# Kernel optimization log

Hardware: AMD Instinct MI355X
Metric: run time of the kernel (lower is better)

The kernel has to match this reference:

```python
import jax, jax.numpy as jnp
import numpy as np

NUM_CLASS = 3
SCORE_THRESH = 0.1
NMS_THRESH = 0.25
PRE = 512    # NMS_PRE_MAXSIZE (reduced from 4096 for memory; same algorithm)
POST = 100   # NMS_POST_MAXSIZE
EPS = 1e-8


def _cross(a, b):
    return a[..., 0] * b[..., 1] - a[..., 1] * b[..., 0]


def _corners(box):
    # box: (7,) = (x, y, z, dx, dy, dz, heading) -> BEV corners (4,2), CCW
    x, y, dx, dy, r = box[0], box[1], box[3], box[4], box[6]
    c, s = jnp.cos(r), jnp.sin(r)
    lx = jnp.array([0.5, -0.5, -0.5, 0.5]) * dx
    ly = jnp.array([0.5, 0.5, -0.5, -0.5]) * dy
    return jnp.stack([x + lx * c - ly * s, y + lx * s + ly * c], axis=-1)


def _in_box(pts, box):
    # pts (P,2): point-in-rotated-rect test in the box frame
    px, py = pts[:, 0] - box[0], pts[:, 1] - box[1]
    c, s = jnp.cos(box[6]), jnp.sin(box[6])
    u = px * c + py * s
    v = -px * s + py * c
    return (jnp.abs(u) <= box[3] * 0.5 + 1e-5) & (jnp.abs(v) <= box[4] * 0.5 + 1e-5)


def _bev_inter_area(ba, bb):
    # Exact rotated-rect intersection area (same construction as the CUDA
    # iou3d kernel: inside corners + edge intersections, angle-sorted shoelace).
    ca, cb = _corners(ba), _corners(bb)
    pa, ra = ca, jnp.roll(ca, -1, 0) - ca       # edges of a
    pb, rb = cb, jnp.roll(cb, -1, 0) - cb       # edges of b
    d = _cross(ra[:, None, :], rb[None, :, :])  # (4,4)
    dsafe = jnp.where(jnp.abs(d) > EPS, d, 1.0)
    qp = pb[None, :, :] - pa[:, None, :]
    t = _cross(qp, rb[None, :, :]) / dsafe
    u = _cross(qp, ra[:, None, :]) / dsafe
    vi = (jnp.abs(d) > EPS) & (t >= 0.0) & (t <= 1.0) & (u >= 0.0) & (u <= 1.0)
    ip = pa[:, None, :] + t[..., None] * ra[:, None, :]  # (4,4,2)
    pts = jnp.concatenate([ca, cb, ip.reshape(16, 2)], 0)          # (24,2)
    val = jnp.concatenate([_in_box(ca, bb), _in_box(cb, ba), vi.reshape(16)], 0)
    cnt = val.sum()
    ctr = (pts * val[:, None]).sum(0) / jnp.maximum(cnt, 1)
    ang = jnp.where(val, jnp.arctan2(pts[:, 1] - ctr[1], pts[:, 0] - ctr[0]), 1e9)
    o = jnp.argsort(ang)
    ps, vs = pts[o], val[o]
    ps = jnp.where(vs[:, None], ps, ps[0])  # collapse invalid onto first valid pt
    area = 0.5 * jnp.abs(_cross(ps, jnp.roll(ps, -1, 0)).sum())
    return jnp.where(cnt >= 3, area, 0.0)


def _iou3d(ba, bb):
    inter = _bev_inter_area(ba, bb)
    zt = jnp.minimum(ba[2] + ba[5] * 0.5, bb[2] + bb[5] * 0.5)
    zb = jnp.maximum(ba[2] - ba[5] * 0.5, bb[2] - bb[5] * 0.5)
    i3 = inter * jnp.maximum(zt - zb, 0.0)
    va = ba[3] * ba[4] * ba[5]
    vb = bb[3] * bb[4] * bb[5]
    return i3 / jnp.maximum(va + vb - i3, EPS)


_iou_mat = jax.vmap(jax.vmap(_iou3d, (None, 0)), (0, None))


def _nms(scores, boxes):
    # scores (K,) sorted descending; greedy suppression in score order
    valid = scores >= SCORE_THRESH
    iou = _iou_mat(boxes, boxes)  # (K,K)

    def body(sup, inp):
        row, v, i = inp
        keep = v & jnp.logical_not(sup[i])
        sup = sup | (keep & (row > NMS_THRESH))
        return sup, keep

    K = scores.shape[0]
    _, keep = jax.lax.scan(body, jnp.zeros((K,), bool), (iou, valid, jnp.arange(K)))
    return keep


def _post_one(cls_logits, boxes):
    # multi_classes_nms path: cls_preds_normalized=False -> sigmoid
    scores = jax.nn.sigmoid(cls_logits)  # (N, NUM_CLASS)
    out_b, out_s, out_l = [], [], []
    for k in range(NUM_CLASS):
        s = jnp.where(scores[:, k] >= SCORE_THRESH, scores[:, k], -1.0)
        top_s, idx = jax.lax.top_k(s, PRE)
        b = boxes[idx]
        keep = _nms(top_s, b)
        ks = jnp.where(keep, top_s, -1.0)
        os_, oi = jax.lax.top_k(ks, POST)
        ov = os_ >= SCORE_THRESH
        out_b.append(jnp.where(ov[:, None], b[oi], 0.0))
        out_s.append(jnp.where(ov, os_, 0.0))
        out_l.append((k + 1) * ov.astype(jnp.int32))  # final_labels = k + 1
    return (jnp.concatenate(out_b, 0), jnp.concatenate(out_s, 0),
            jnp.concatenate(out_l, 0))


def setup_inputs() -> dict:
    key = jax.random.key(0)
    k1, k2 = jax.random.split(key)
    B, N = 2, 100000
    batch_cls_preds = jax.random.normal(k1, (B, N, NUM_CLASS), dtype=jnp.float32)
    u = jax.random.uniform(k2, (B, N, 7), dtype=jnp.float32)
    x = u[..., 0] * 70.0
    y = u[..., 1] * 80.0 - 40.0
    z = u[..., 2] * 2.0 - 1.0
    dx = u[..., 3] * 3.0 + 1.5
    dy = u[..., 4] * 1.5 + 1.2
    dz = u[..., 5] * 1.0 + 1.3
    r = u[..., 6] * 2.0 * np.pi - np.pi
    batch_box_preds = jnp.stack([x, y, z, dx, dy, dz, r], axis=-1)
    return {"batch_cls_preds": batch_cls_preds, "batch_box_preds": batch_box_preds}


def reference(batch_cls_preds, batch_box_preds):
    # returns per-batch padded (pred_boxes (B, 3*POST, 7), pred_scores, pred_labels);
    # invalid slots are zeroed (label 0 == no detection)
    return jax.vmap(_post_one)(batch_cls_preds, batch_box_preds)
```

## Files before the change

### kernel.cpp

```cpp
#include <hip/hip_runtime.h>
#include <cstdint>

#define NCLS 3
#define NPTS 100000
#define NB 2
#define PRE 512
#define POST 100
#define SCORE_TH 0.1f
#define NMS_TH 0.25
#define CAP 1024
#define NBINS 384
#define XBIN_SH 16
#define XBIN_OFF (0xBFC00000u >> XBIN_SH)
#define XMARG 2e-3f
#define NPROB (NB * NCLS)
#define CPB 4
#define NKB 25
#define BUFREG 1024
#define BUFSZ (NKB * BUFREG)
#define NCELL 36
#define GEOP 21
#define NRB 1024
#define RB_OFF (0xBF400000u >> 12)


__device__ __forceinline__ uint32_t score_key(float x)
{
    double sd = 1.0 / (1.0 + exp(-(double)x));
    float s = (float)sd;
    if (!(s >= SCORE_TH)) s = -1.0f;
    uint32_t u = __float_as_uint(s);
    return (u & 0x80000000u) ? ~u : (u | 0x80000000u);
}

__device__ __forceinline__ int xbin(float x)
{
    uint32_t u = __float_as_uint(x);
    uint32_t key = (u & 0x80000000u) ? ~u : (u | 0x80000000u);
    int b = (int)(key >> XBIN_SH) - (int)XBIN_OFF;
    return b < 0 ? 0 : (b > NBINS - 1 ? NBINS - 1 : b);
}

__global__ __launch_bounds__(1024) void hist_stage_kernel(
    const float* __restrict__ cls, uint32_t* __restrict__ hist_part,
    uint32_t* __restrict__ blkcnt, unsigned long long* __restrict__ buf)
{
    __shared__ uint32_t lh[NCLS][NBINS];
    __shared__ uint32_t lcnt3[NCLS];
    const int tid = threadIdx.x;
    for (int t = tid; t < NCLS * NBINS; t += 1024) ((uint32_t*)lh)[t] = 0;
    if (tid < NCLS) lcnt3[tid] = 0;
    __syncthreads();

    const int b = blockIdx.x / NKB, kb = blockIdx.x % NKB;
    const float* base = cls + (size_t)b * NPTS * NCLS;
    #pragma unroll
    for (int c = 0; c < CPB; ++c) {
        int i = (kb * CPB + c) * 1024 + tid;
        if (i < NPTS) {
            const float* cp = base + (size_t)i * NCLS;
            #pragma unroll
            for (int k = 0; k < NCLS; ++k) {
                float x = cp[k];
                int bn = xbin(x);
                if (bn > 0) atomicAdd(&lh[k][bn], 1u);
                if (xbin(x + XMARG) >= 1) {
                    uint32_t slot = atomicAdd(&lcnt3[k], 1u);
                    if (slot < BUFREG)
                        buf[(size_t)(b * NCLS + k) * BUFSZ + kb * BUFREG + slot]
                            = ((unsigned long long)__float_as_uint(x) << 32)
                            | (uint32_t)i;
                }
            }
        }
    }
    __syncthreads();
    for (int t = tid; t < NCLS * NBINS; t += 1024) {
        int k = t / NBINS, bin = t % NBINS;
        hist_part[((size_t)(b * NCLS + k) * NBINS + bin) * NKB + kb]
            = lh[k][bin];
    }
    if (tid < NCLS) {
        uint32_t c = lcnt3[tid];
        blkcnt[(b * NKB + kb) * NCLS + tid] = c < BUFREG ? c : BUFREG;
    }
}

__global__ __launch_bounds__(1024) void cell_kernel(
    const float* __restrict__ boxes, const uint32_t* __restrict__ hist_part,
    const uint32_t* __restrict__ blkcnt,
    const unsigned long long* __restrict__ buf,
    uint32_t* __restrict__ cand_idx, float* __restrict__ cand_score,
    unsigned long long* __restrict__ mask)
{
    const int blk = blockIdx.x;
    const int p = blk / NCELL;
    const int b = p / NCLS, k = p % NCLS;
    int cc = blk % NCELL;
    int wi = 0;
    while (cc >= 8 - wi) { cc -= 8 - wi; ++wi; }
    const int wj = wi + cc;
    const int tid = threadIdx.x;
    const int lane = tid & 63;
    const int wv = tid >> 6;

    __shared__ unsigned long long skey[CAP];
    __shared__ unsigned long long skey2[CAP];
    __shared__ uint32_t sbins[NBINS];
    __shared__ uint32_t sblk[NKB];
    __shared__ uint32_t rhist[NRB + 1];
    __shared__ uint32_t rcnt[NRB];
    __shared__ double geo[128][GEOP];
    __shared__ float scx[128], scy[128];
    __shared__ float sczlo[128], sczhi[128], scrad[128];
    __shared__ uint32_t lcnt;

    for (int t = tid; t < 128 * GEOP; t += 1024) ((double*)geo)[t] = 0.0;
    rhist[tid] = 0;
    rcnt[tid] = 0;
    if (tid == 0) { rhist[NRB] = 0; lcnt = 0; }
    if (tid < 128) {
        scx[tid] = 0.0f; scy[tid] = 0.0f;
        sczlo[tid] = 0.0f; sczhi[tid] = 0.0f; scrad[tid] = 0.0f;
    }
    if (wi == 0 && wj == 0 && tid < PRE) {
        cand_idx[p * PRE + tid] = 0;
        cand_score[p * PRE + tid] = -1.0f;
    }
    if (tid < NKB) sblk[tid] = blkcnt[(b * NKB + tid) * NCLS + k];
    if (tid < NBINS) {
        const uint32_t* bp2 = hist_part
            + ((size_t)(b * NCLS + k) * NBINS + tid) * NKB;
        uint32_t s = 0;
        #pragma unroll 5
        for (int kb = 0; kb < NKB; ++kb)
            s += bp2[kb];
        sbins[tid] = s;
    }
    __syncthreads();

    int pb;
    {
        int pbw = -1;
        uint32_t carry = 0;
        #pragma unroll
        for (int c = 5; c >= 0; --c) {
            uint32_t v = sbins[c * 64 + lane];
            #pragma unroll
            for (int off = 1; off < 64; off <<= 1) {
                uint32_t o = __shfl_down(v, off);
                v += (lane + off < 64) ? o : 0u;
            }
            uint32_t full = v + carry;
            unsigned long long bal = __ballot(full >= PRE);
            if (pbw < 0 && bal)
                pbw = c * 64 + (63 - __clzll((long long)bal));
            carry += (uint32_t)__shfl((int)v, 0);
        }
        pb = pbw < 1 ? 1 : pbw;
    }

    {
        const int q = tid >> 8;
        const int slot0 = tid & 255;
        for (int r0 = 0; r0 < NKB; r0 += 4) {
            const int r = r0 + q;
            if (r < NKB) {
                const uint32_t c_r = sblk[r];
                const unsigned long long* R =
                    buf + (size_t)p * BUFSZ + r * BUFREG;
                for (uint32_t t = (uint32_t)slot0; t < c_r; t += 256) {
                    unsigned long long e = R[t];
                    float x = __uint_as_float((uint32_t)(e >> 32));
                    uint32_t i = (uint32_t)e;
                    if (xbin(x + XMARG) >= pb) {
                        uint32_t kk = score_key(x);
                        uint32_t slot = atomicAdd(&lcnt, 1u);
                        if (slot < CAP)
                            skey[slot] = ((unsigned long long)kk << 32)
                                       | (uint32_t)(~i);
                    }
                }
            }
        }
    }
    __syncthreads();
    const int cnt = (int)(lcnt < CAP ? lcnt : CAP);

    unsigned long long mykey = (tid < cnt) ? skey[tid] : 0ull;
    int myrb = 0;
    if (tid < cnt) {
        uint32_t kk = (uint32_t)(mykey >> 32);
        int v = (int)(kk >> 12) - (int)RB_OFF;
        myrb = v < 0 ? 0 : (v > NRB - 1 ? NRB - 1 : v);
        atomicAdd(&rhist[myrb], 1u);
    }
    __syncthreads();

    if (wv == 0) {
        uint32_t carry = 0;
        for (int c = (NRB / 64) - 1; c >= 0; --c) {
            uint32_t v = rhist[c * 64 + lane];
            uint32_t sfx = v;
            #pragma unroll
            for (int off = 1; off < 64; off <<= 1) {
                uint32_t o = __shfl_down(sfx, off);
                sfx += (lane + off < 64) ? o : 0u;
            }
            rhist[c * 64 + lane] = sfx + carry;
            carry += (uint32_t)__shfl((int)sfx, 0);
        }
    }
    __syncthreads();

    int mylo = 0;
    if (tid < cnt) {
        mylo = (int)rhist[myrb + 1];
        uint32_t off = atomicAdd(&rcnt[myrb], 1u);
        skey2[mylo + off] = mykey;
    }
    __syncthreads();

    int rank = 0;
    if (tid < cnt) {
        const int hi2 = (int)rhist[myrb];
        int c2 = 0;
        for (int t = mylo; t < hi2; ++t)
            c2 += (skey2[t] > mykey) ? 1 : 0;
        rank = mylo + c2;
    }

    if (tid < cnt) {
        uint32_t idx = ~((uint32_t)mykey);
        if (wi == 0 && wj == 0 && rank < PRE) {
            uint32_t ov = (uint32_t)(mykey >> 32);
            uint32_t ub = (ov & 0x80000000u) ? (ov ^ 0x80000000u) : ~ov;
            cand_idx[p * PRE + rank] = idx;
            cand_score[p * PRE + rank] = __uint_as_float(ub);
        }
        const int slotA = rank - wi * 64;
        const int slotB = rank - wj * 64;
        const bool inA = (slotA >= 0 && slotA < 64);
        const bool inB = (slotB >= 0 && slotB < 64);
        if (inA || inB) {
            const float* bp = boxes + ((size_t)b * NPTS + idx) * 7;
            double x = bp[0], y = bp[1], z = bp[2];
            double dx = bp[3], dy = bp[4], dz = bp[5], r = bp[6];
            double c = cos(r), s = sin(r);
            double hx = 0.5 * dx, hy = 0.5 * dy;
            double zlo = z - 0.5 * dz, zhi = z + 0.5 * dz;
            double rad = sqrt(hx * hx + hy * hy);
            double V[20];
            V[0] = x; V[1] = y; V[2] = c; V[3] = s; V[4] = hx; V[5] = hy;
            V[6] = zlo; V[7] = zhi; V[8] = dx * dy * dz; V[9] = rad;
            const double lxs[4] = { hx, -hx, -hx,  hx };
            const double lys[4] = { hy,  hy, -hy, -hy };
            #pragma unroll
            for (int m = 0; m < 4; ++m) {
                V[10 + m] = x + lxs[m] * c - lys[m] * s;
                V[14 + m] = y + lxs[m] * s + lys[m] * c;
            }
            if (inA) {
                #pragma unroll
                for (int m = 0; m < 20; ++m) geo[slotA][m] = V[m];
                scx[slotA] = (float)x; scy[slotA] = (float)y;
                sczlo[slotA] = (float)zlo; sczhi[slotA] = (float)zhi;
                scrad[slotA] = (float)rad;
            }
            if (inB) {
                #pragma unroll
                for (int m = 0; m < 20; ++m) geo[64 + slotB][m] = V[m];
                scx[64 + slotB] = (float)x; scy[64 + slotB] = (float)y;
                sczlo[64 + slotB] = (float)zlo; sczhi[64 + slotB] = (float)zhi;
                scrad[64 + slotB] = (float)rad;
            }
        }
    }
    __syncthreads();

    const int half = lane >> 5;
    const int lane31 = lane & 31;
    for (int rr = wv; rr < 64; rr += 16) {
        const int bi = wi * 64 + rr;
        const double* A = geo[rr];

        bool needPoly = false;
        {
            const int jcol = wj * 64 + lane;
            if (jcol > bi) {
                float hzf = fminf(sczhi[rr], sczhi[64 + lane])
                          - fmaxf(sczlo[rr], sczlo[64 + lane]);
                if (hzf > 0.0f) {
                    float ddxf = scx[rr] - scx[64 + lane];
                    float ddyf = scy[rr] - scy[64 + lane];
                    float rsf = scrad[rr] + scrad[64 + lane] + 0.01f;
                    if (ddxf * ddxf + ddyf * ddyf <= rsf * rsf) {
                        const double* B = geo[64 + lane];
                        double hzd = fmin(A[7], B[7]) - fmax(A[6], B[6]);
                        if (hzd > 0.0) {
                            double ddx = B[0] - A[0], ddy = B[1] - A[1];
                            double ca = A[2], sa = A[3];
                            double cb2 = B[2], sb2 = B[3];
                            double cd = fabs(ca * cb2 + sa * sb2);
                            double sd = fabs(sa * cb2 - ca * sb2);
                            double pax = fabs(ddx * ca + ddy * sa);
                            double pay = fabs(-ddx * sa + ddy * ca);
                            double pbx = fabs(ddx * cb2 + ddy * sb2);
                            double pby = fabs(-ddx * sb2 + ddy * cb2);
                            if (!(pax > A[4] + B[4] * cd + B[5] * sd) &&
                                !(pay > A[5] + B[4] * sd + B[5] * cd) &&
                                !(pbx > B[4] + A[4] * cd + A[5] * sd) &&
                                !(pby > B[5] + A[4] * sd + A[5] * cd)) {
                                double areaA = 4.0 * A[4] * A[5];
                                double areaB = 4.0 * B[4] * B[5];
                                double i3m = fmin(areaA, areaB) * hzd;
                                double den = A[8] + B[8] - i3m;
                                if (den < 1e-8) den = 1e-8;
                                needPoly = (i3m / den > (double)NMS_TH);
                            }
                        }
                    }
                }
            }
        }
        unsigned long long pmask = __ballot(needPoly);
        unsigned long long supw = 0ull;

        while (pmask) {
            int jb0 = __ffsll(pmask) - 1;
            unsigned long long pm1 = pmask & (pmask - 1ull);
            int jb1 = pm1 ? (__ffsll(pm1) - 1) : -1;
            pmask = pm1 ? (pm1 & (pm1 - 1ull)) : 0ull;
            const int jb = half ? jb1 : jb0;
            const bool act = jb >= 0;
            const double* B = geo[64 + (act ? jb : 0)];

            double PX = 0.0, PY = 0.0;
            bool valid = false;
            if (act) {
                if (lane31 < 8) {
                    const double* S = (lane31 < 4) ? A : B;
                    const double* O = (lane31 < 4) ? B : A;
                    int m = lane31 & 3;
                    PX = S[10 + m]; PY = S[14 + m];
                    double rx = PX - O[0], ry = PY - O[1];
                    double u =  rx * O[2] + ry * O[3];
                    double v = -rx * O[3] + ry * O[2];
                    valid = (fabs(u) <= O[4] + 1e-5) && (fabs(v) <= O[5] + 1e-5);
                } else if (lane31 < 24) {
                    int e = lane31 - 8, m = e >> 2, nn = e & 3;
                    double ax = A[10 + m], ay = A[14 + m];
                    double rax = A[10 + ((m + 1) & 3)] - ax;
                    double ray = A[14 + ((m + 1) & 3)] - ay;
                    double bx = B[10 + nn], by = B[14 + nn];
                    double rbx = B[10 + ((nn + 1) & 3)] - bx;
                    double rby = B[14 + ((nn + 1) & 3)] - by;
                    double d = rax * rby - ray * rbx;
                    if (fabs(d) > 1e-8) {
                        double qx = bx - ax, qy = by - ay;
                        double tt = (qx * rby - qy * rbx) / d;
                        double uu = (qx * ray - qy * rax) / d;
                        valid = (tt >= 0.0 && tt <= 1.0 && uu >= 0.0 && uu <= 1.0);
                        PX = ax + tt * rax; PY = ay + tt * ray;
                    }
                }
            }
            if (!valid) { PX = 0.0; PY = 0.0; }

            unsigned long long bal = __ballot(valid);
            int cntv = __popc((uint32_t)(bal >> (half ? 32 : 0)));
            double sx = PX, sy = PY;
            #pragma unroll
            for (int off = 16; off; off >>= 1) {
                sx += __shfl_xor(sx, off);
                sy += __shfl_xor(sy, off);
            }
            int cdiv = cntv > 0 ? cntv : 1;
            double cxc = sx / cdiv, cyc = sy / cdiv;

            double ang = valid ? atan2(PY - cyc, PX - cxc) : 1e9;
            int sidx = lane31;

            #pragma unroll
            for (int kk2 = 2; kk2 <= 32; kk2 <<= 1) {
                #pragma unroll
                for (int jj = kk2 >> 1; jj > 0; jj >>= 1) {
                    double oang = __shfl_xor(ang, jj);
                    double opx  = __shfl_xor(PX, jj);
                    double opy  = __shfl_xor(PY, jj);
                    int    oidx = __shfl_xor(sidx, jj);
                    bool iLow = (lane31 & jj) == 0;
                    bool dirUp = (lane31 & kk2) == 0;
                    bool mineFirst = (ang < oang) || (ang == oang && sidx < oidx);
                    bool keepMine = (mineFirst == (iLow == dirUp));
                    if (!keepMine) { ang = oang; PX = opx; PY = opy; sidx = oidx; }
                }
            }

            double nxp = __shfl(PX, (half << 5) | ((lane31 + 1) & 31));
            double nyp = __shfl(PY, (half << 5) | ((lane31 + 1) & 31));
            double fx  = __shfl(PX, half << 5);
            double fy  = __shfl(PY, half << 5);
            bool last = (lane31 == cntv - 1);
            double qx = last ? fx : nxp, qy = last ? fy : nyp;
            double contrib = 0.0;
            if (lane31 < cntv)
                contrib = (PX - cxc) * (qy - cyc) - (PY - cyc) * (qx - cxc);
            #pragma unroll
            for (int off = 16; off; off >>= 1)
                contrib += __shfl_xor(contrib, off);
            double inter = (cntv >= 3) ? 0.5 * fabs(contrib) : 0.0;

            if (act && lane31 == 0) {
                double zt = fmin(A[7], B[7]);
                double zb = fmax(A[6], B[6]);
                double hz = zt - zb;
                bool sup = false;
                if (hz > 0.0) {
                    double i3 = inter * hz;
                    double den = A[8] + B[8] - i3;
                    if (den < 1e-8) den = 1e-8;
                    sup = (i3 / den) > (double)NMS_TH;
                }
                if (sup) supw |= 1ull << jb;
            }
        }

        supw |= __shfl_xor(supw, 32);
        if (lane == 0)
            mask[(size_t)(p * PRE + bi) * 8 + wj] = supw;
    }
}

__global__ __launch_bounds__(256) void nms_out_kernel(
    const float* __restrict__ boxes, const uint32_t* __restrict__ cand_idx,
    const float* __restrict__ cand_score,
    const unsigned long long* __restrict__ mask, float* __restrict__ out)
{
    const int p = blockIdx.x;
    const int b = p / NCLS, k = p % NCLS;
    const int tid = threadIdx.x;

    __shared__ unsigned long long smask[PRE * 8];
    __shared__ float sscore[PRE];
    __shared__ int slist[POST];
    __shared__ int scnt;

    for (int w = tid; w < PRE * 8; w += 256)
        smask[w] = mask[(size_t)p * PRE * 8 + w];
    for (int i = tid; i < PRE; i += 256)
        sscore[i] = cand_score[p * PRE + i];
    __syncthreads();

    if (tid < 64) {
        const int ln = tid;
        unsigned long long rem = 0ull;
        #pragma unroll
        for (int w = 0; w < 8; ++w) {
            unsigned long long bw = __ballot(sscore[w * 64 + ln] >= SCORE_TH);
            if (ln == w) rem = bw;
        }
        int c = 0;
        for (;;) {
            int cv = rem ? ((ln << 6) + (__ffsll(rem) - 1)) : 4096;
            int o1 = __shfl_xor(cv, 1); cv = cv < o1 ? cv : o1;
            int o2 = __shfl_xor(cv, 2); cv = cv < o2 ? cv : o2;
            int o4 = __shfl_xor(cv, 4); cv = cv < o4 ? cv : o4;
            int i = __shfl(cv, 0);
            if (i >= 4096) break;
            if (ln == 0) slist[c] = i;
            ++c;
            if (c >= POST) break;
            unsigned long long mm = (ln < 8) ? smask[i * 8 + ln] : 0ull;
            if (ln == (i >> 6)) mm |= 1ull << (i & 63);
            rem &= ~mm;
        }
        if (ln == 0) scnt = c;
    }
    __syncthreads();

    const int cnt2 = scnt;
    for (int t2 = tid; t2 < POST; t2 += 256) {
        int row = b * (NCLS * POST) + k * POST + t2;
        float* ob = out + (size_t)row * 7;
        float* os = out + (size_t)NB * NCLS * POST * 7 + row;
        float* ol = out + (size_t)NB * NCLS * POST * 7 + (size_t)NB * NCLS * POST + row;
        if (t2 < cnt2) {
            int rr = slist[t2];
            uint32_t idx = cand_idx[p * PRE + rr];
            const float* bp = boxes + ((size_t)b * NPTS + idx) * 7;
            #pragma unroll
            for (int c7 = 0; c7 < 7; ++c7) ob[c7] = bp[c7];
            *os = sscore[rr];
            *ol = (float)(k + 1);
        } else {
            #pragma unroll
            for (int c7 = 0; c7 < 7; ++c7) ob[c7] = 0.0f;
            *os = 0.0f;
            *ol = 0.0f;
        }
    }
}

extern "C" void kernel_launch(void* const* d_in, const int* in_sizes, int n_in,
                              void* d_out, int out_size, void* d_ws, size_t ws_size,
                              hipStream_t stream)
{
    (void)in_sizes; (void)n_in; (void)out_size; (void)ws_size;
    const float* cls   = (const float*)d_in[0];
    const float* boxes = (const float*)d_in[1];
    float* out = (float*)d_out;

    char* ws = (char*)d_ws;
    uint32_t* hist_part   = (uint32_t*)(ws);
    uint32_t* blkcnt      = (uint32_t*)(ws + 230400);
    unsigned long long* buf = (unsigned long long*)(ws + 231424);
    uint32_t* cand_idx    = (uint32_t*)(ws + 1460224);
    float*    cand_score  = (float*)   (ws + 1472512);
    unsigned long long* mask = (unsigned long long*)(ws + 1484800);

    hipLaunchKernelGGL(hist_stage_kernel, dim3(NB * NKB), dim3(1024), 0,
                       stream, cls, hist_part, blkcnt, buf);
    hipLaunchKernelGGL(cell_kernel, dim3(NPROB * NCELL), dim3(1024), 0,
                       stream, boxes, hist_part, blkcnt, buf,
                       cand_idx, cand_score, mask);
    hipLaunchKernelGGL(nms_out_kernel, dim3(NPROB), dim3(256), 0, stream,
                       boxes, cand_idx, cand_score, mask, out);
}
```

Before: 127.4 us.

## Use more histogram blocks and queue polygon IoU pairs across half-waves

The histogram stage now has each block handle one 1024-point chunk, giving 98 blocks per batch instead of 25, which spreads the streaming pass over more CUs. The buffer bound check is dropped because a region can no longer overflow. In the cell kernel, pairs that need exact polygon intersection are compacted into a shared-memory queue and spread evenly over all half-waves, and results are merged with shared atomicOr. This replaces the per-row loop, where warps with many candidate pairs left others idle. The cost is larger hist_part reads in cell_kernel, plus extra atomics and a barrier.

```diff
diff --git a/kernel.cpp b/kernel.cpp
--- a/kernel.cpp
+++ b/kernel.cpp
@@ -14,8 +14,7 @@
 #define XBIN_OFF (0xBFC00000u >> XBIN_SH)
 #define XMARG 2e-3f
 #define NPROB (NB * NCLS)
-#define CPB 4
-#define NKB 25
+#define NKB 98
 #define BUFREG 1024
 #define BUFSZ (NKB * BUFREG)
 #define NCELL 36
@@ -53,24 +52,19 @@
     __syncthreads();
 
     const int b = blockIdx.x / NKB, kb = blockIdx.x % NKB;
-    const float* base = cls + (size_t)b * NPTS * NCLS;
-    #pragma unroll
-    for (int c = 0; c < CPB; ++c) {
-        int i = (kb * CPB + c) * 1024 + tid;
-        if (i < NPTS) {
-            const float* cp = base + (size_t)i * NCLS;
-            #pragma unroll
-            for (int k = 0; k < NCLS; ++k) {
-                float x = cp[k];
-                int bn = xbin(x);
-                if (bn > 0) atomicAdd(&lh[k][bn], 1u);
-                if (xbin(x + XMARG) >= 1) {
-                    uint32_t slot = atomicAdd(&lcnt3[k], 1u);
-                    if (slot < BUFREG)
-                        buf[(size_t)(b * NCLS + k) * BUFSZ + kb * BUFREG + slot]
-                            = ((unsigned long long)__float_as_uint(x) << 32)
-                            | (uint32_t)i;
-                }
+    const int i = kb * 1024 + tid;
+    if (i < NPTS) {
+        const float* cp = cls + ((size_t)b * NPTS + i) * NCLS;
+        #pragma unroll
+        for (int k = 0; k < NCLS; ++k) {
+            float x = cp[k];
+            int bn = xbin(x);
+            if (bn > 0) atomicAdd(&lh[k][bn], 1u);
+            if (xbin(x + XMARG) >= 1) {
+                uint32_t slot = atomicAdd(&lcnt3[k], 1u);
+                buf[(size_t)(b * NCLS + k) * BUFSZ + kb * BUFREG + slot]
+                    = ((unsigned long long)__float_as_uint(x) << 32)
+                    | (uint32_t)i;
             }
         }
     }
@@ -80,10 +74,8 @@
         hist_part[((size_t)(b * NCLS + k) * NBINS + bin) * NKB + kb]
             = lh[k][bin];
     }
-    if (tid < NCLS) {
-        uint32_t c = lcnt3[tid];
-        blkcnt[(b * NKB + kb) * NCLS + tid] = c < BUFREG ? c : BUFREG;
-    }
+    if (tid < NCLS)
+        blkcnt[(b * NKB + kb) * NCLS + tid] = lcnt3[tid];
 }
 
 __global__ __launch_bounds__(1024) void cell_kernel(
@@ -104,8 +96,10 @@
     const int lane = tid & 63;
     const int wv = tid >> 6;
 
-    __shared__ unsigned long long skey[CAP];
-    __shared__ unsigned long long skey2[CAP];
+    __shared__ unsigned long long skeybuf[2 * CAP];
+    unsigned long long* skey  = skeybuf;
+    unsigned long long* skey2 = skeybuf + CAP;
+    uint32_t* queue = (uint32_t*)skeybuf;
     __shared__ uint32_t sbins[NBINS];
     __shared__ uint32_t sblk[NKB];
     __shared__ uint32_t rhist[NRB + 1];
@@ -113,6 +107,7 @@
     __shared__ double geo[128][GEOP];
     __shared__ float scx[128], scy[128];
     __shared__ float sczlo[128], sczhi[128], scrad[128];
+    __shared__ uint32_t smw[128];
     __shared__ uint32_t lcnt;
 
     for (int t = tid; t < 128 * GEOP; t += 1024) ((double*)geo)[t] = 0.0;
@@ -122,6 +117,7 @@
     if (tid < 128) {
         scx[tid] = 0.0f; scy[tid] = 0.0f;
         sczlo[tid] = 0.0f; sczhi[tid] = 0.0f; scrad[tid] = 0.0f;
+        smw[tid] = 0u;
     }
     if (wi == 0 && wj == 0 && tid < PRE) {
         cand_idx[p * PRE + tid] = 0;
@@ -132,7 +128,7 @@
         const uint32_t* bp2 = hist_part
             + ((size_t)(b * NCLS + k) * NBINS + tid) * NKB;
         uint32_t s = 0;
-        #pragma unroll 5
+        #pragma unroll 7
         for (int kb = 0; kb < NKB; ++kb)
             s += bp2[kb];
         sbins[tid] = s;
@@ -161,15 +157,15 @@
     }
 
     {
-        const int q = tid >> 8;
-        const int slot0 = tid & 255;
-        for (int r0 = 0; r0 < NKB; r0 += 4) {
-            const int r = r0 + q;
+        const int rsub = tid >> 6;
+        const int slot0 = tid & 63;
+        for (int r0 = 0; r0 < NKB; r0 += 16) {
+            const int r = r0 + rsub;
             if (r < NKB) {
                 const uint32_t c_r = sblk[r];
                 const unsigned long long* R =
                     buf + (size_t)p * BUFSZ + r * BUFREG;
-                for (uint32_t t = (uint32_t)slot0; t < c_r; t += 256) {
+                for (uint32_t t = (uint32_t)slot0; t < c_r; t += 64) {
                     unsigned long long e = R[t];
                     float x = __uint_as_float((uint32_t)(e >> 32));
                     uint32_t i = (uint32_t)e;
@@ -196,6 +192,7 @@
         atomicAdd(&rhist[myrb], 1u);
     }
     __syncthreads();
+    if (tid == 0) lcnt = 0;
 
     if (wv == 0) {
         uint32_t carry = 0;
@@ -278,12 +275,9 @@
     }
     __syncthreads();
 
-    const int half = lane >> 5;
-    const int lane31 = lane & 31;
     for (int rr = wv; rr < 64; rr += 16) {
         const int bi = wi * 64 + rr;
         const double* A = geo[rr];
-
         bool needPoly = false;
         {
             const int jcol = wj * 64 + lane;
@@ -323,112 +317,123 @@
                 }
             }
         }
-        unsigned long long pmask = __ballot(needPoly);
-        unsigned long long supw = 0ull;
-
-        while (pmask) {
-            int jb0 = __ffsll(pmask) - 1;
-            unsigned long long pm1 = pmask & (pmask - 1ull);
-            int jb1 = pm1 ? (__ffsll(pm1) - 1) : -1;
-            pmask = pm1 ? (pm1 & (pm1 - 1ull)) : 0ull;
-            const int jb = half ? jb1 : jb0;
-            const bool act = jb >= 0;
-            const double* B = geo[64 + (act ? jb : 0)];
-
-            double PX = 0.0, PY = 0.0;
-            bool valid = false;
-            if (act) {
-                if (lane31 < 8) {
-                    const double* S = (lane31 < 4) ? A : B;
-                    const double* O = (lane31 < 4) ? B : A;
-                    int m = lane31 & 3;
-                    PX = S[10 + m]; PY = S[14 + m];
-                    double rx = PX - O[0], ry = PY - O[1];
-                    double u =  rx * O[2] + ry * O[3];
-                    double v = -rx * O[3] + ry * O[2];
-                    valid = (fabs(u) <= O[4] + 1e-5) && (fabs(v) <= O[5] + 1e-5);
-                } else if (lane31 < 24) {
-                    int e = lane31 - 8, m = e >> 2, nn = e & 3;
-                    double ax = A[10 + m], ay = A[14 + m];
-                    double rax = A[10 + ((m + 1) & 3)] - ax;
-                    double ray = A[14 + ((m + 1) & 3)] - ay;
-                    double bx = B[10 + nn], by = B[14 + nn];
-                    double rbx = B[10 + ((nn + 1) & 3)] - bx;
-                    double rby = B[14 + ((nn + 1) & 3)] - by;
-                    double d = rax * rby - ray * rbx;
-                    if (fabs(d) > 1e-8) {
-                        double qx = bx - ax, qy = by - ay;
-                        double tt = (qx * rby - qy * rbx) / d;
-                        double uu = (qx * ray - qy * rax) / d;
-                        valid = (tt >= 0.0 && tt <= 1.0 && uu >= 0.0 && uu <= 1.0);
-                        PX = ax + tt * rax; PY = ay + tt * ray;
-                    }
+        if (needPoly) {
+            uint32_t pos = atomicAdd(&lcnt, 1u);
+            queue[pos] = (uint32_t)((rr << 6) | lane);
+        }
+    }
+    __syncthreads();
+    const int qcnt = (int)lcnt;
+
+    const int half = lane >> 5;
+    const int lane31 = lane & 31;
+    const int hid = (wv << 1) | half;
+    for (int base = 0; base < qcnt; base += 32) {
+        const int qi = base + hid;
+        const bool act = qi < qcnt;
+        uint32_t e = act ? queue[qi] : 0u;
+        const int rr_ = (int)(e >> 6) & 63;
+        const int jb = (int)(e & 63u);
+        const double* A = geo[rr_];
+        const double* B = geo[64 + jb];
+
+        double PX = 0.0, PY = 0.0;
+        bool valid = false;
+        if (act) {
+            if (lane31 < 8) {
+                const double* S = (lane31 < 4) ? A : B;
+                const double* O = (lane31 < 4) ? B : A;
+                int m = lane31 & 3;
+                PX = S[10 + m]; PY = S[14 + m];
+                double rx = PX - O[0], ry = PY - O[1];
+                double u =  rx * O[2] + ry * O[3];
+                double v = -rx * O[3] + ry * O[2];
+                valid = (fabs(u) <= O[4] + 1e-5) && (fabs(v) <= O[5] + 1e-5);
+            } else if (lane31 < 24) {
+                int e2 = lane31 - 8, m = e2 >> 2, nn = e2 & 3;
+                double ax = A[10 + m], ay = A[14 + m];
+                double rax = A[10 + ((m + 1) & 3)] - ax;
+                double ray = A[14 + ((m + 1) & 3)] - ay;
+                double bx = B[10 + nn], by = B[14 + nn];
+                double rbx = B[10 + ((nn + 1) & 3)] - bx;
+                double rby = B[14 + ((nn + 1) & 3)] - by;
+                double d = rax * rby - ray * rbx;
+                if (fabs(d) > 1e-8) {
+                    double qx = bx - ax, qy = by - ay;
+                    double tt = (qx * rby - qy * rbx) / d;
+                    double uu = (qx * ray - qy * rax) / d;
+                    valid = (tt >= 0.0 && tt <= 1.0 && uu >= 0.0 && uu <= 1.0);
+                    PX = ax + tt * rax; PY = ay + tt * ray;
                 }
             }
-            if (!valid) { PX = 0.0; PY = 0.0; }
-
-            unsigned long long bal = __ballot(valid);
-            int cntv = __popc((uint32_t)(bal >> (half ? 32 : 0)));
-            double sx = PX, sy = PY;
+        }
+        if (!valid) { PX = 0.0; PY = 0.0; }
+
+        unsigned long long bal = __ballot(valid);
+        int cntv = __popc((uint32_t)(bal >> (half ? 32 : 0)));
+        double sx = PX, sy = PY;
+        #pragma unroll
+        for (int off = 16; off; off >>= 1) {
+            sx += __shfl_xor(sx, off);
+            sy += __shfl_xor(sy, off);
+        }
+        int cdiv = cntv > 0 ? cntv : 1;
+        double cxc = sx / cdiv, cyc = sy / cdiv;
+
+        double ang = valid ? atan2(PY - cyc, PX - cxc) : 1e9;
+        int sidx = lane31;
+
+        #pragma unroll
+        for (int kk2 = 2; kk2 <= 32; kk2 <<= 1) {
             #pragma unroll
-            for (int off = 16; off; off >>= 1) {
-                sx += __shfl_xor(sx, off);
-                sy += __shfl_xor(sy, off);
-            }
-            int cdiv = cntv > 0 ? cntv : 1;
-            double cxc = sx / cdiv, cyc = sy / cdiv;
-
-            double ang = valid ? atan2(PY - cyc, PX - cxc) : 1e9;
-            int sidx = lane31;
-
-            #pragma unroll
-            for (int kk2 = 2; kk2 <= 32; kk2 <<= 1) {
-                #pragma unroll
-                for (int jj = kk2 >> 1; jj > 0; jj >>= 1) {
-                    double oang = __shfl_xor(ang, jj);
-                    double opx  = __shfl_xor(PX, jj);
-                    double opy  = __shfl_xor(PY, jj);
-                    int    oidx = __shfl_xor(sidx, jj);
-                    bool iLow = (lane31 & jj) == 0;
-                    bool dirUp = (lane31 & kk2) == 0;
-                    bool mineFirst = (ang < oang) || (ang == oang && sidx < oidx);
-                    bool keepMine = (mineFirst == (iLow == dirUp));
-                    if (!keepMine) { ang = oang; PX = opx; PY = opy; sidx = oidx; }
-                }
-            }
-
-            double nxp = __shfl(PX, (half << 5) | ((lane31 + 1) & 31));
-            double nyp = __shfl(PY, (half << 5) | ((lane31 + 1) & 31));
-            double fx  = __shfl(PX, half << 5);
-            double fy  = __shfl(PY, half << 5);
-            bool last = (lane31 == cntv - 1);
-            double qx = last ? fx : nxp, qy = last ? fy : nyp;
-            double contrib = 0.0;
-            if (lane31 < cntv)
-                contrib = (PX - cxc) * (qy - cyc) - (PY - cyc) * (qx - cxc);
-            #pragma unroll
-            for (int off = 16; off; off >>= 1)
-                contrib += __shfl_xor(contrib, off);
-            double inter = (cntv >= 3) ? 0.5 * fabs(contrib) : 0.0;
-
-            if (act && lane31 == 0) {
-                double zt = fmin(A[7], B[7]);
-                double zb = fmax(A[6], B[6]);
-                double hz = zt - zb;
-                bool sup = false;
-                if (hz > 0.0) {
-                    double i3 = inter * hz;
-                    double den = A[8] + B[8] - i3;
-                    if (den < 1e-8) den = 1e-8;
-                    sup = (i3 / den) > (double)NMS_TH;
-                }
-                if (sup) supw |= 1ull << jb;
-            }
-        }
-
-        supw |= __shfl_xor(supw, 32);
-        if (lane == 0)
-            mask[(size_t)(p * PRE + bi) * 8 + wj] = supw;
+            for (int jj = kk2 >> 1; jj > 0; jj >>= 1) {
+                double oang = __shfl_xor(ang, jj);
+                double opx  = __shfl_xor(PX, jj);
+                double opy  = __shfl_xor(PY, jj);
+                int    oidx = __shfl_xor(sidx, jj);
+                bool iLow = (lane31 & jj) == 0;
+                bool dirUp = (lane31 & kk2) == 0;
+                bool mineFirst = (ang < oang) || (ang == oang && sidx < oidx);
+                bool keepMine = (mineFirst == (iLow == dirUp));
+                if (!keepMine) { ang = oang; PX = opx; PY = opy; sidx = oidx; }
+            }
+        }
+
+        double nxp = __shfl(PX, (half << 5) | ((lane31 + 1) & 31));
+        double nyp = __shfl(PY, (half << 5) | ((lane31 + 1) & 31));
+        double fx  = __shfl(PX, half << 5);
+        double fy  = __shfl(PY, half << 5);
+        bool last = (lane31 == cntv - 1);
+        double qx = last ? fx : nxp, qy = last ? fy : nyp;
+        double contrib = 0.0;
+        if (lane31 < cntv)
+            contrib = (PX - cxc) * (qy - cyc) - (PY - cyc) * (qx - cxc);
+        #pragma unroll
+        for (int off = 16; off; off >>= 1)
+            contrib += __shfl_xor(contrib, off);
+        double inter = (cntv >= 3) ? 0.5 * fabs(contrib) : 0.0;
+
+        if (act && lane31 == 0) {
+            double zt = fmin(A[7], B[7]);
+            double zb = fmax(A[6], B[6]);
+            double hz = zt - zb;
+            bool sup = false;
+            if (hz > 0.0) {
+                double i3 = inter * hz;
+                double den = A[8] + B[8] - i3;
+                if (den < 1e-8) den = 1e-8;
+                sup = (i3 / den) > (double)NMS_TH;
+            }
+            if (sup)
+                atomicOr(&smw[rr_ * 2 + (jb >> 5)], 1u << (jb & 31));
+        }
+    }
+    __syncthreads();
+
+    if (tid < 64) {
+        unsigned long long w = (unsigned long long)smw[tid * 2]
+            | ((unsigned long long)smw[tid * 2 + 1] << 32);
+        mask[(size_t)(p * PRE + wi * 64 + tid) * 8 + wj] = w;
     }
 }
 
@@ -513,11 +518,11 @@
 
     char* ws = (char*)d_ws;
     uint32_t* hist_part   = (uint32_t*)(ws);
-    uint32_t* blkcnt      = (uint32_t*)(ws + 230400);
-    unsigned long long* buf = (unsigned long long*)(ws + 231424);
-    uint32_t* cand_idx    = (uint32_t*)(ws + 1460224);
-    float*    cand_score  = (float*)   (ws + 1472512);
-    unsigned long long* mask = (unsigned long long*)(ws + 1484800);
+    uint32_t* blkcnt      = (uint32_t*)(ws + 903168);
+    unsigned long long* buf = (unsigned long long*)(ws + 905600);
+    uint32_t* cand_idx    = (uint32_t*)(ws + 5722496);
+    float*    cand_score  = (float*)   (ws + 5734784);
+    unsigned long long* mask = (unsigned long long*)(ws + 5747072);
 
     hipLaunchKernelGGL(hist_stage_kernel, dim3(NB * NKB), dim3(1024), 0,
                        stream, cls, hist_part, blkcnt, buf);
```

Measured after the change: 123.5 us. 3.0% less time.
